# Kernel optimization log

Measured on AMD Instinct MI355X. Metric: run time of the kernel, lower is better.

Reference implementation:

```python
import jax, jax.numpy as jnp
import numpy as np


def _gru_cell(x, h, Wih, Whh):
    # PyTorch GRU (bias=False): gates ordered [r, z, n] along rows of W.
    gi = x @ Wih.T              # [B, 3H]
    gh = h @ Whh.T              # [B, 3H]
    ir, iz, inn = jnp.split(gi, 3, axis=-1)
    hr, hz, hn = jnp.split(gh, 3, axis=-1)
    r = jax.nn.sigmoid(ir + hr)
    z = jax.nn.sigmoid(iz + hz)
    n = jnp.tanh(inn + r * hn)
    return (1.0 - z) * n + z * h


def setup_inputs() -> dict:
    key = jax.random.key(0)
    ks = jax.random.split(key, 16)
    B, T = 256, 1024
    U, Z, Y, H = 16, 16, 16, 128
    W = 0.1  # weight scale for stable recurrence
    inp = {
        "u": jax.random.normal(ks[0], (B, U, T), jnp.float32),
        "y": jax.random.normal(ks[1], (B, Y, T), jnp.float32),
        "h0": jax.random.uniform(ks[2], (2, B, H), jnp.float32),
        "Wih0": W * jax.random.normal(ks[3], (3 * H, U + Z), jnp.float32),
        "Whh0": W * jax.random.normal(ks[4], (3 * H, H), jnp.float32),
        "Wih1": W * jax.random.normal(ks[5], (3 * H, H), jnp.float32),
        "Whh1": W * jax.random.normal(ks[6], (3 * H, H), jnp.float32),
        "dW1": W * jax.random.normal(ks[7], (H, U + H), jnp.float32),
        "db1": jnp.zeros((H,), jnp.float32),
        "dW2": W * jax.random.normal(ks[8], (Z, H), jnp.float32),
        "db2": jnp.zeros((Z,), jnp.float32),
        "mW1": W * jax.random.normal(ks[9], (H, Z + H), jnp.float32),
        "mb1": jnp.zeros((H,), jnp.float32),
        "mW2": W * jax.random.normal(ks[10], (H, H), jnp.float32),
        "mb2": jnp.zeros((H,), jnp.float32),
        "mW3": W * jax.random.normal(ks[11], (Y, H), jnp.float32),
        "mb3": jnp.zeros((Y,), jnp.float32),
    }
    return inp


def reference(u, y, h0, Wih0, Whh0, Wih1, Whh1,
              dW1, db1, dW2, db2, mW1, mb1, mW2, mb2, mW3, mb3):
    B, Z = u.shape[0], dW2.shape[0]
    u_t = jnp.transpose(u, (2, 0, 1))  # [T, B, U]
    y_t = jnp.transpose(y, (2, 0, 1))  # [T, B, Y]

    def step(carry, xs):
        h, x_prev, loss = carry  # h: [2, B, H]
        ut, yt = xs
        inp = jnp.concatenate([ut, x_prev], axis=1)       # [B, U+Z]
        h0n = _gru_cell(inp, h[0], Wih0, Whh0)
        h1n = _gru_cell(h0n, h[1], Wih1, Whh1)
        h_new = jnp.stack([h0n, h1n], axis=0)
        # dynn: two Linears, no activation; input cat(u_t, h[-1])
        d_in = jnp.concatenate([ut, h1n], axis=1)         # [B, U+H]
        x_t = (d_in @ dW1.T + db1) @ dW2.T + db2          # [B, Z]
        # menn: Linear -> ReLU -> Linear -> Linear; input cat(x_t, h[0])
        m_in = jnp.concatenate([x_t, h0n], axis=1)        # [B, Z+H]
        m = jax.nn.relu(m_in @ mW1.T + mb1)
        m = m @ mW2.T + mb2
        y_hat = m @ mW3.T + mb3                           # [B, Y]
        loss = loss + jnp.sum((y_hat - yt) ** 2)
        return (h_new, x_t, loss), None

    x0 = jnp.zeros((B, Z), jnp.float32)  # x_tm1 at t=0 is zeros
    (_, _, loss), _ = jax.lax.scan(step, (h0, x0, jnp.float32(0.0)), (u_t, y_t))
    return loss
```

## Files before the change

kernel.cpp:

```cpp
#include <hip/hip_runtime.h>

typedef __bf16 bf16x8 __attribute__((ext_vector_type(8)));
typedef float f32x4 __attribute__((ext_vector_type(4)));
typedef unsigned int uint32;
typedef unsigned short ushort16_t;

#define T_STEPS 1024
#define CHUNK 32

#define H0_OFF   0
#define H1_OFF   8704
#define M1_OFF   17408
#define XB_OFF   21760
#define ZP_OFF   22528
#define UCH_OFF  22592
#define YCH_OFF  47168
#define WL_OFF   71744
#define LDS_BYTES 146496

#define TG0 0
#define TG1 24
#define TG2 120
#define TG3 216
#define TG4 312
#define TG5 317
#define TG6 357
#define NT_TOT 361
#define SC_DC  369664
#define SC_ME  378880
#define SC_DBC 387072
#define SC_MBE 387136

static __device__ __forceinline__ ushort16_t f2bf(float f) {
    uint32 u = __builtin_bit_cast(uint32, f);
    return (ushort16_t)((u + 0x7FFFu + ((u >> 16) & 1u)) >> 16);
}
static __device__ __forceinline__ float bf2f(ushort16_t h) {
    uint32 u = ((uint32)h) << 16;
    return __builtin_bit_cast(float, u);
}
static __device__ __forceinline__ float sigm(float x) { return 1.f / (1.f + __expf(-x)); }
static __device__ __forceinline__ float tanh_fast(float x) {
    x = fmaxf(fminf(x, 30.f), -30.f);
    float e = __expf(-2.f * x);
    return (1.f - e) / (1.f + e);
}
static __device__ __forceinline__ f32x4 mfma16(bf16x8 a, bf16x8 b, f32x4 c) {
    return __builtin_amdgcn_mfma_f32_16x16x32_bf16(a, b, c, 0, 0, 0);
}
static __device__ __forceinline__ bf16x8 ldsAF(const char* p) {
    return __builtin_bit_cast(bf16x8, *(const uint4*)p);
}

__global__ void prep1(const float* __restrict__ dW1, const float* __restrict__ db1,
                      const float* __restrict__ dW2, const float* __restrict__ db2,
                      const float* __restrict__ mW2, const float* __restrict__ mb2,
                      const float* __restrict__ mW3, const float* __restrict__ mb3,
                      char* __restrict__ ws, float* __restrict__ out) {
    int id = blockIdx.x * 256 + threadIdx.x;
    if (id == 0) *out = 0.f;
    if (id < 2304) {
        int n = id / 144, k = id % 144;
        float s = 0.f;
        for (int h = 0; h < 128; ++h) s += dW2[n * 128 + h] * dW1[h * 144 + k];
        ((float*)(ws + SC_DC))[id] = s;
    } else if (id < 4352) {
        int e = id - 2304, n = e / 128, k = e % 128;
        float s = 0.f;
        for (int h = 0; h < 128; ++h) s += mW3[n * 128 + h] * mW2[h * 128 + k];
        ((float*)(ws + SC_ME))[e] = s;
    } else if (id < 4368) {
        int n = id - 4352;
        float s = db2[n];
        for (int h = 0; h < 128; ++h) s += dW2[n * 128 + h] * db1[h];
        ((float*)(ws + SC_DBC))[n] = s;
    } else if (id < 4384) {
        int n = id - 4368;
        float s = mb3[n];
        for (int h = 0; h < 128; ++h) s += mW3[n * 128 + h] * mb2[h];
        ((float*)(ws + SC_MBE))[n] = s;
    }
}

__global__ void prep2(const float* __restrict__ W0, const float* __restrict__ W1,
                      const float* __restrict__ W2, const float* __restrict__ W3,
                      const float* __restrict__ W5, char* __restrict__ ws) {
    const int tt = blockIdx.x;
    const int lane = threadIdx.x;
    const int cum[8] = {TG0, TG1, TG2, TG3, TG4, TG5, TG6, NT_TOT};
    const int Kreal[7] = {32, 128, 128, 128, 144, 144, 128};
    const int KT[7] = {1, 4, 4, 4, 5, 5, 4};
    const float* Ws[7] = {W0, W1, W2, W3, (const float*)(ws + SC_DC), W5, (const float*)(ws + SC_ME)};
    int g = 0;
    while (tt >= cum[g + 1]) ++g;
    const int tl = tt - cum[g];
    const int kt = tl % KT[g];
    const int n = (tl / KT[g]) * 16 + (lane & 15);
    const float* W = Ws[g];
    ushort16_t* o = (ushort16_t*)ws + tt * 512 + lane * 8;
#pragma unroll
    for (int j = 0; j < 8; ++j) {
        int k = kt * 32 + (lane >> 4) * 8 + j;
        o[j] = (k < Kreal[g]) ? f2bf(W[n * Kreal[g] + k]) : (ushort16_t)0;
    }
}

__global__ __launch_bounds__(512, 2) void rnn_main(
    const float* __restrict__ u, const float* __restrict__ yg, const float* __restrict__ h0g,
    const char* __restrict__ ws, const float* __restrict__ mb1g,
    const float* __restrict__ dbCg, const float* __restrict__ mbEg,
    float* __restrict__ out) {
    __shared__ __align__(16) char smem[LDS_BYTES];
    const int tid = threadIdx.x;
    const int lane = tid & 63;
    const int w = tid >> 6;
    const int lr = lane & 15;
    const int lg = lane >> 4;
    const int r0 = blockIdx.x * 16;
    const uint4* F4 = (const uint4*)ws;
    const f32x4 zero = {0.f, 0.f, 0.f, 0.f};

    for (int i = tid; i < (768 + 64) / 4; i += 512) *(uint32*)(smem + XB_OFF + i * 4) = 0;
    for (int i = tid; i < 1024; i += 512) {
        int lay = i >> 9, rem = i & 511, rr = rem >> 5, k4 = rem & 31;
        float4 v = *(const float4*)(h0g + (lay * 256 + r0 + rr) * 128 + k4 * 4);
        uint2 pk;
        pk.x = (uint32)f2bf(v.x) | ((uint32)f2bf(v.y) << 16);
        pk.y = (uint32)f2bf(v.z) | ((uint32)f2bf(v.w) << 16);
        *(uint2*)(smem + H0_OFF + lay * 8704 + rr * 272 + k4 * 8) = pk;
    }
    for (int i = tid; i < 73 * 64; i += 512) {
        int li = i >> 6, ln2 = i & 63;
        int gt2 = (li < 24) ? li : (li < 29) ? TG4 + (li - 24) : (li < 69) ? TG5 + (li - 29) : TG6 + (li - 69);
        *((uint4*)(smem + WL_OFF) + i) = F4[gt2 * 64 + ln2];
    }
    __syncthreads();

    bf16x8 wW[3][3][4];
    for (int p = 0; p < 6; ++p) {
        for (int i = tid; i < 3072; i += 512)
            *((uint4*)(smem + UCH_OFF) + i) = F4[(TG1 + p * 48) * 64 + i];
        __syncthreads();
#pragma unroll
        for (int mat = 0; mat < 3; ++mat)
#pragma unroll
            for (int gg = 0; gg < 3; ++gg) {
                int rel0 = mat * 96 + gg * 32 + w * 4;
                if (rel0 >= p * 48 && rel0 < p * 48 + 48) {
#pragma unroll
                    for (int kt = 0; kt < 4; ++kt)
                        wW[mat][gg][kt] = ldsAF(smem + UCH_OFF + (rel0 - p * 48 + kt) * 1024 + lane * 16);
                }
            }
        __syncthreads();
    }

    const float mb1_c = mb1g[w * 16 + lr];
    const float dbC_l = dbCg[lr];
    const float mbE_l = mbEg[lr];
    float loss = 0.f;

    const int r = lr;
    for (int t = 0; t <= T_STEPS; ++t) {
        const int cur = t & 1, nxt = cur ^ 1;
        const char* h0c = smem + H0_OFF + cur * 4352;
        char* h0n = smem + H0_OFF + nxt * 4352;
        const char* h1c = smem + H1_OFF + cur * 4352;
        char* h1n = smem + H1_OFF + nxt * 4352;
        const int s = t & (CHUNK - 1);

        if ((t & (CHUNK - 1)) == 0) {
            if (t < T_STEPS) {
                for (int q = 0; q < 16; ++q) {
                    int pair = w * 32 + q * 2 + (lane >> 5);
                    int rr2 = pair >> 4, ch = pair & 15, ss = lane & 31;
                    float v = u[(r0 + rr2) * 16384 + ch * 1024 + t + ss];
                    *(ushort16_t*)(smem + UCH_OFF + ss * 768 + rr2 * 48 + ch * 2) = f2bf(v);
                }
            }
            for (int q = 0; q < 16; ++q) {
                int pair = w * 32 + q * 2 + (lane >> 5);
                int rr2 = pair >> 4, ch = pair & 15, ss = lane & 31;
                int gt = t - 1 + ss;
                if (gt >= 0 && gt < T_STEPS) {
                    float v = yg[(r0 + rr2) * 16384 + ch * 1024 + gt];
                    *(ushort16_t*)(smem + YCH_OFF + ss * 768 + rr2 * 48 + ch * 2) = f2bf(v);
                }
            }
            __syncthreads();
        }

        if (t < T_STEPS) {
            const char* ainp_p = (lg < 2) ? (smem + UCH_OFF + s * 768 + r * 48 + lg * 16)
                                          : (smem + XB_OFF + r * 48 + (lg - 2) * 16);
            bf16x8 a_inp = ldsAF(ainp_p);
            bf16x8 ah[4];
#pragma unroll
            for (int kt = 0; kt < 4; ++kt) ah[kt] = ldsAF(h0c + r * 272 + kt * 64 + lg * 16);
            f32x4 aRi = mfma16(a_inp, ldsAF(smem + WL_OFF + (0 * 8 + w) * 1024 + lane * 16), zero);
            f32x4 aZi = mfma16(a_inp, ldsAF(smem + WL_OFF + (1 * 8 + w) * 1024 + lane * 16), zero);
            f32x4 aNi = mfma16(a_inp, ldsAF(smem + WL_OFF + (2 * 8 + w) * 1024 + lane * 16), zero);
            f32x4 aRh = zero, aZh = zero, aNh = zero;
#pragma unroll
            for (int kt = 0; kt < 4; ++kt) {
                aRh = mfma16(ah[kt], wW[0][0][kt], aRh);
                aZh = mfma16(ah[kt], wW[0][1][kt], aZh);
                aNh = mfma16(ah[kt], wW[0][2][kt], aNh);
            }
            const int c = w * 16 + lr;
#pragma unroll
            for (int i = 0; i < 4; ++i) {
                int row = lg * 4 + i;
                float hold = bf2f(*(const ushort16_t*)(h0c + row * 272 + c * 2));
                float rr = sigm(aRi[i] + aRh[i]);
                float zz = sigm(aZi[i] + aZh[i]);
                float nn = tanh_fast(aNi[i] + rr * aNh[i]);
                *(ushort16_t*)(h0n + row * 272 + c * 2) = f2bf((1.f - zz) * nn + zz * hold);
            }
        }
        if (t > 0) {
            bf16x8 am[5];
            am[0] = ldsAF((lg < 2) ? (smem + XB_OFF + r * 48 + lg * 16) : (h0c + r * 272 + (lg - 2) * 16));
#pragma unroll
            for (int kt = 1; kt < 4; ++kt) am[kt] = ldsAF(h0c + r * 272 + kt * 64 - 32 + lg * 16);
            am[4] = ldsAF((lg < 2) ? (h0c + r * 272 + 224 + lg * 16) : (smem + ZP_OFF + (lg - 2) * 16));
            f32x4 m = zero;
#pragma unroll
            for (int kt = 0; kt < 5; ++kt)
                m = mfma16(am[kt], ldsAF(smem + WL_OFF + (29 + w * 5 + kt) * 1024 + lane * 16), m);
#pragma unroll
            for (int i = 0; i < 4; ++i) {
                int row = lg * 4 + i;
                *(ushort16_t*)(smem + M1_OFF + row * 272 + (w * 16 + lr) * 2) =
                    f2bf(fmaxf(m[i] + mb1_c, 0.f));
            }
        }
        __syncthreads();

        if (t < T_STEPS) {
            bf16x8 ag[4], ahh[4];
#pragma unroll
            for (int kt = 0; kt < 4; ++kt) {
                ag[kt] = ldsAF(h0n + r * 272 + kt * 64 + lg * 16);
                ahh[kt] = ldsAF(h1c + r * 272 + kt * 64 + lg * 16);
            }
            f32x4 bRi = zero, bRh = zero, bZi = zero, bZh = zero, bNi = zero, bNh = zero;
#pragma unroll
            for (int kt = 0; kt < 4; ++kt) {
                bRi = mfma16(ag[kt], wW[1][0][kt], bRi);
                bRh = mfma16(ahh[kt], wW[2][0][kt], bRh);
                bZi = mfma16(ag[kt], wW[1][1][kt], bZi);
                bZh = mfma16(ahh[kt], wW[2][1][kt], bZh);
                bNi = mfma16(ag[kt], wW[1][2][kt], bNi);
                bNh = mfma16(ahh[kt], wW[2][2][kt], bNh);
            }
            const int c = w * 16 + lr;
#pragma unroll
            for (int i = 0; i < 4; ++i) {
                int row = lg * 4 + i;
                float hold = bf2f(*(const ushort16_t*)(h1c + row * 272 + c * 2));
                float rr = sigm(bRi[i] + bRh[i]);
                float zz = sigm(bZi[i] + bZh[i]);
                float nn = tanh_fast(bNi[i] + rr * bNh[i]);
                *(ushort16_t*)(h1n + row * 272 + c * 2) = f2bf((1.f - zz) * nn + zz * hold);
            }
        }
        if (t > 0 && w == 7) {
            bf16x8 am1[4];
#pragma unroll
            for (int kt = 0; kt < 4; ++kt) am1[kt] = ldsAF(smem + M1_OFF + r * 272 + kt * 64 + lg * 16);
            f32x4 acc = zero;
#pragma unroll
            for (int kt = 0; kt < 4; ++kt)
                acc = mfma16(am1[kt], ldsAF(smem + WL_OFF + (69 + kt) * 1024 + lane * 16), acc);
#pragma unroll
            for (int i = 0; i < 4; ++i) {
                int row = lg * 4 + i;
                float yv = bf2f(*(const ushort16_t*)(smem + YCH_OFF + s * 768 + row * 48 + lr * 2));
                float d = acc[i] + mbE_l - yv;
                loss += d * d;
            }
        }
        __syncthreads();

        if (t < T_STEPS && w == 0) {
            bf16x8 ad[5];
            ad[0] = ldsAF((lg < 2) ? (smem + UCH_OFF + s * 768 + r * 48 + lg * 16)
                                   : (h1n + r * 272 + (lg - 2) * 16));
#pragma unroll
            for (int kt = 1; kt < 4; ++kt) ad[kt] = ldsAF(h1n + r * 272 + kt * 64 - 32 + lg * 16);
            ad[4] = ldsAF((lg < 2) ? (h1n + r * 272 + 224 + lg * 16) : (smem + ZP_OFF + (lg - 2) * 16));
            f32x4 acc = zero;
#pragma unroll
            for (int kt = 0; kt < 5; ++kt)
                acc = mfma16(ad[kt], ldsAF(smem + WL_OFF + (24 + kt) * 1024 + lane * 16), acc);
#pragma unroll
            for (int i = 0; i < 4; ++i) {
                int row = lg * 4 + i;
                *(ushort16_t*)(smem + XB_OFF + row * 48 + lr * 2) = f2bf(acc[i] + dbC_l);
            }
        }
        __syncthreads();
    }

    if (w == 7) {
#pragma unroll
        for (int off = 32; off > 0; off >>= 1) loss += __shfl_down(loss, off, 64);
        if (lane == 0) atomicAdd(out, loss);
    }
}

extern "C" void kernel_launch(void* const* d_in, const int* in_sizes, int n_in,
                              void* d_out, int out_size, void* d_ws, size_t ws_size,
                              hipStream_t stream) {
    const float* u    = (const float*)d_in[0];
    const float* y    = (const float*)d_in[1];
    const float* h0   = (const float*)d_in[2];
    const float* Wih0 = (const float*)d_in[3];
    const float* Whh0 = (const float*)d_in[4];
    const float* Wih1 = (const float*)d_in[5];
    const float* Whh1 = (const float*)d_in[6];
    const float* dW1  = (const float*)d_in[7];
    const float* db1  = (const float*)d_in[8];
    const float* dW2  = (const float*)d_in[9];
    const float* db2  = (const float*)d_in[10];
    const float* mW1  = (const float*)d_in[11];
    const float* mb1  = (const float*)d_in[12];
    const float* mW2  = (const float*)d_in[13];
    const float* mb2  = (const float*)d_in[14];
    const float* mW3  = (const float*)d_in[15];
    const float* mb3  = (const float*)d_in[16];
    float* out = (float*)d_out;
    char* ws = (char*)d_ws;

    prep1<<<dim3(18), dim3(256), 0, stream>>>(dW1, db1, dW2, db2, mW2, mb2, mW3, mb3, ws, out);
    prep2<<<dim3(NT_TOT), dim3(64), 0, stream>>>(Wih0, Whh0, Wih1, Whh1, mW1, ws);
    rnn_main<<<dim3(16), dim3(512), 0, stream>>>(u, y, h0, ws, mb1,
                                                 (const float*)(ws + SC_DBC),
                                                 (const float*)(ws + SC_MBE), out);
}
```

Before: 3.327 ms.

## Compute dynn output redundantly per wave via MFMA and lane permute, dropping a barrier

Every wave now recomputes the small dynn projection x_t from the previous h1 with a transposed MFMA and redistributes it through ds_bpermute. This removes the wave-0-only stage and one of the three block barriers per timestep. The menn first layer is moved into the same phase as the layer-0 GRU, and the previous hidden state is kept in fp32 registers instead of being reloaded from LDS. The change also adds faster exp2/rcp sigmoid and tanh, packed bf16 conversion, and split accumulators that shorten MFMA dependency chains. The cost is redundant MFMA work in each wave and an epilogue that handles the final step separately.

```diff
diff --git a/kernel.cpp b/kernel.cpp
--- a/kernel.cpp
+++ b/kernel.cpp
@@ -3,20 +3,17 @@
 typedef __bf16 bf16x8 __attribute__((ext_vector_type(8)));
 typedef float f32x4 __attribute__((ext_vector_type(4)));
 typedef unsigned int uint32;
-typedef unsigned short ushort16_t;
+typedef unsigned short u16;
 
 #define T_STEPS 1024
-#define CHUNK 32
 
 #define H0_OFF   0
 #define H1_OFF   8704
 #define M1_OFF   17408
-#define XB_OFF   21760
-#define ZP_OFF   22528
-#define UCH_OFF  22592
-#define YCH_OFF  47168
-#define WL_OFF   71744
-#define LDS_BYTES 146496
+#define UCH_OFF  21760
+#define YCH_OFF  46336
+#define WL_OFF   70912
+#define LDS_BYTES 145664
 
 #define TG0 0
 #define TG1 24
@@ -31,19 +28,26 @@
 #define SC_DBC 387072
 #define SC_MBE 387136
 
-static __device__ __forceinline__ ushort16_t f2bf(float f) {
+static __device__ __forceinline__ u16 f2bf(float f) {
     uint32 u = __builtin_bit_cast(uint32, f);
-    return (ushort16_t)((u + 0x7FFFu + ((u >> 16) & 1u)) >> 16);
-}
-static __device__ __forceinline__ float bf2f(ushort16_t h) {
+    return (u16)((u + 0x7FFFu + ((u >> 16) & 1u)) >> 16);
+}
+static __device__ __forceinline__ float bf2f(u16 h) {
     uint32 u = ((uint32)h) << 16;
     return __builtin_bit_cast(float, u);
 }
-static __device__ __forceinline__ float sigm(float x) { return 1.f / (1.f + __expf(-x)); }
+static __device__ __forceinline__ uint32 cvtpk(float a, float b) {
+    uint32 r;
+    asm("v_cvt_pk_bf16_f32 %0, %1, %2" : "=v"(r) : "v"(a), "v"(b));
+    return r;
+}
+static __device__ __forceinline__ float sigm(float x) {
+    return __builtin_amdgcn_rcpf(1.f + __builtin_amdgcn_exp2f(x * -1.4426950408889634f));
+}
 static __device__ __forceinline__ float tanh_fast(float x) {
-    x = fmaxf(fminf(x, 30.f), -30.f);
-    float e = __expf(-2.f * x);
-    return (1.f - e) / (1.f + e);
+    float xm = fmaxf(x, -30.f);
+    float e = __builtin_amdgcn_exp2f(xm * -2.8853900817779268f);
+    return fmaf(2.f, __builtin_amdgcn_rcpf(e + 1.f), -1.f);
 }
 static __device__ __forceinline__ f32x4 mfma16(bf16x8 a, bf16x8 b, f32x4 c) {
     return __builtin_amdgcn_mfma_f32_16x16x32_bf16(a, b, c, 0, 0, 0);
@@ -97,11 +101,11 @@
     const int kt = tl % KT[g];
     const int n = (tl / KT[g]) * 16 + (lane & 15);
     const float* W = Ws[g];
-    ushort16_t* o = (ushort16_t*)ws + tt * 512 + lane * 8;
+    u16* o = (u16*)ws + tt * 512 + lane * 8;
 #pragma unroll
     for (int j = 0; j < 8; ++j) {
         int k = kt * 32 + (lane >> 4) * 8 + j;
-        o[j] = (k < Kreal[g]) ? f2bf(W[n * Kreal[g] + k]) : (ushort16_t)0;
+        o[j] = (k < Kreal[g]) ? f2bf(W[n * Kreal[g] + k]) : (u16)0;
     }
 }
 
@@ -119,8 +123,8 @@
     const int r0 = blockIdx.x * 16;
     const uint4* F4 = (const uint4*)ws;
     const f32x4 zero = {0.f, 0.f, 0.f, 0.f};
-
-    for (int i = tid; i < (768 + 64) / 4; i += 512) *(uint32*)(smem + XB_OFF + i * 4) = 0;
+    const bf16x8 z8 = __builtin_bit_cast(bf16x8, (uint4){0u, 0u, 0u, 0u});
+
     for (int i = tid; i < 1024; i += 512) {
         int lay = i >> 9, rem = i & 511, rr = rem >> 5, k4 = rem & 31;
         float4 v = *(const float4*)(h0g + (lay * 256 + r0 + rr) * 128 + k4 * 4);
@@ -156,27 +160,56 @@
     }
 
     const float mb1_c = mb1g[w * 16 + lr];
-    const float dbC_l = dbCg[lr];
     const float mbE_l = mbEg[lr];
+    float dbc4[4];
+#pragma unroll
+    for (int i = 0; i < 4; ++i) dbc4[i] = dbCg[lg * 4 + i];
+    float hp0[4], hp1[4];
+#pragma unroll
+    for (int i = 0; i < 4; ++i) {
+        hp0[i] = h0g[(r0 + lg * 4 + i) * 128 + w * 16 + lr];
+        hp1[i] = h0g[(256 + r0 + lg * 4 + i) * 128 + w * 16 + lr];
+    }
     float loss = 0.f;
-
-    const int r = lr;
-    for (int t = 0; t <= T_STEPS; ++t) {
-        const int cur = t & 1, nxt = cur ^ 1;
-        const char* h0c = smem + H0_OFF + cur * 4352;
-        char* h0n = smem + H0_OFF + nxt * 4352;
-        const char* h1c = smem + H1_OFF + cur * 4352;
-        char* h1n = smem + H1_OFF + nxt * 4352;
-        const int s = t & (CHUNK - 1);
-
-        if ((t & (CHUNK - 1)) == 0) {
-            if (t < T_STEPS) {
-                for (int q = 0; q < 16; ++q) {
-                    int pair = w * 32 + q * 2 + (lane >> 5);
-                    int rr2 = pair >> 4, ch = pair & 15, ss = lane & 31;
-                    float v = u[(r0 + rr2) * 16384 + ch * 1024 + t + ss];
-                    *(ushort16_t*)(smem + UCH_OFF + ss * 768 + rr2 * 48 + ch * 2) = f2bf(v);
-                }
+    const int c2 = (w * 16 + lr) * 2;
+    const int bp0 = (lr + (lg & 1) * 32) * 4;
+
+    for (int t = 0; t < T_STEPS; ++t) {
+        const char* h0c = smem + H0_OFF + (t & 1) * 4352;
+        char* h0n = smem + H0_OFF + ((t & 1) ^ 1) * 4352;
+        const char* h1c = smem + H1_OFF + (t & 1) * 4352;
+        char* h1n = smem + H1_OFF + ((t & 1) ^ 1) * 4352;
+        const int s = t & 31, sp = (t - 1) & 31;
+
+        const char* h1r = h1c + lr * 272;
+        bf16x8 ad0 = ldsAF((lg < 2) ? (smem + UCH_OFF + sp * 768 + lr * 48 + lg * 16)
+                                    : (h1r + (lg - 2) * 16));
+        bf16x8 ad1 = ldsAF(h1r + 32 + lg * 16);
+        bf16x8 ad2 = ldsAF(h1r + 96 + lg * 16);
+        bf16x8 ad3 = ldsAF(h1r + 160 + lg * 16);
+        bf16x8 ad4t = ldsAF(h1r + 224 + (lg & 1) * 16);
+        bf16x8 ad4 = (lg < 2) ? ad4t : z8;
+        f32x4 xa = mfma16(ldsAF(smem + WL_OFF + 24 * 1024 + lane * 16), ad0, zero);
+        xa = mfma16(ldsAF(smem + WL_OFF + 25 * 1024 + lane * 16), ad1, xa);
+        xa = mfma16(ldsAF(smem + WL_OFF + 26 * 1024 + lane * 16), ad2, xa);
+        f32x4 xb = mfma16(ldsAF(smem + WL_OFF + 27 * 1024 + lane * 16), ad3, zero);
+        xb = mfma16(ldsAF(smem + WL_OFF + 28 * 1024 + lane * 16), ad4, xb);
+        uint32 pk0 = cvtpk(xa[0] + xb[0] + dbc4[0], xa[1] + xb[1] + dbc4[1]);
+        uint32 pk1 = cvtpk(xa[2] + xb[2] + dbc4[2], xa[3] + xb[3] + dbc4[3]);
+        if (t == 0) { pk0 = 0u; pk1 = 0u; }
+        uint32 d0 = (uint32)__builtin_amdgcn_ds_bpermute(bp0, (int)pk0);
+        uint32 d1 = (uint32)__builtin_amdgcn_ds_bpermute(bp0, (int)pk1);
+        uint32 d2 = (uint32)__builtin_amdgcn_ds_bpermute(bp0 + 64, (int)pk0);
+        uint32 d3 = (uint32)__builtin_amdgcn_ds_bpermute(bp0 + 64, (int)pk1);
+        bf16x8 xfrag = __builtin_bit_cast(bf16x8, (uint4){d0, d1, d2, d3});
+
+        if ((t & 31) == 0) {
+            __syncthreads();
+            for (int q = 0; q < 16; ++q) {
+                int pair = w * 32 + q * 2 + (lane >> 5);
+                int rr2 = pair >> 4, ch = pair & 15, ss = lane & 31;
+                float v = u[(r0 + rr2) * 16384 + ch * 1024 + t + ss];
+                *(u16*)(smem + UCH_OFF + ss * 768 + rr2 * 48 + ch * 2) = f2bf(v);
             }
             for (int q = 0; q < 16; ++q) {
                 int pair = w * 32 + q * 2 + (lane >> 5);
@@ -184,123 +217,186 @@
                 int gt = t - 1 + ss;
                 if (gt >= 0 && gt < T_STEPS) {
                     float v = yg[(r0 + rr2) * 16384 + ch * 1024 + gt];
-                    *(ushort16_t*)(smem + YCH_OFF + ss * 768 + rr2 * 48 + ch * 2) = f2bf(v);
+                    *(u16*)(smem + YCH_OFF + ss * 768 + rr2 * 48 + ch * 2) = f2bf(v);
                 }
             }
             __syncthreads();
         }
 
-        if (t < T_STEPS) {
-            const char* ainp_p = (lg < 2) ? (smem + UCH_OFF + s * 768 + r * 48 + lg * 16)
-                                          : (smem + XB_OFF + r * 48 + (lg - 2) * 16);
-            bf16x8 a_inp = ldsAF(ainp_p);
-            bf16x8 ah[4];
-#pragma unroll
-            for (int kt = 0; kt < 4; ++kt) ah[kt] = ldsAF(h0c + r * 272 + kt * 64 + lg * 16);
-            f32x4 aRi = mfma16(a_inp, ldsAF(smem + WL_OFF + (0 * 8 + w) * 1024 + lane * 16), zero);
-            f32x4 aZi = mfma16(a_inp, ldsAF(smem + WL_OFF + (1 * 8 + w) * 1024 + lane * 16), zero);
-            f32x4 aNi = mfma16(a_inp, ldsAF(smem + WL_OFF + (2 * 8 + w) * 1024 + lane * 16), zero);
-            f32x4 aRh = zero, aZh = zero, aNh = zero;
-#pragma unroll
-            for (int kt = 0; kt < 4; ++kt) {
-                aRh = mfma16(ah[kt], wW[0][0][kt], aRh);
-                aZh = mfma16(ah[kt], wW[0][1][kt], aZh);
-                aNh = mfma16(ah[kt], wW[0][2][kt], aNh);
+        bf16x8 ufrag = ldsAF(smem + UCH_OFF + s * 768 + lr * 48 + (lg & 1) * 16);
+        bf16x8 a_inp = (lg < 2) ? ufrag : xfrag;
+        const char* h0r = h0c + lr * 272;
+        bf16x8 ah0 = ldsAF(h0r + lg * 16);
+        bf16x8 ah1 = ldsAF(h0r + 64 + lg * 16);
+        bf16x8 ah2 = ldsAF(h0r + 128 + lg * 16);
+        bf16x8 ah3 = ldsAF(h0r + 192 + lg * 16);
+        bf16x8 b0r = ldsAF(smem + WL_OFF + (0 * 8 + w) * 1024 + lane * 16);
+        bf16x8 b0z = ldsAF(smem + WL_OFF + (1 * 8 + w) * 1024 + lane * 16);
+        bf16x8 b0n = ldsAF(smem + WL_OFF + (2 * 8 + w) * 1024 + lane * 16);
+        f32x4 rA = mfma16(ah0, wW[0][0][0], zero);
+        rA = mfma16(ah1, wW[0][0][1], rA);
+        rA = mfma16(a_inp, b0r, rA);
+        f32x4 rB = mfma16(ah2, wW[0][0][2], zero);
+        rB = mfma16(ah3, wW[0][0][3], rB);
+        f32x4 zA = mfma16(ah0, wW[0][1][0], zero);
+        zA = mfma16(ah1, wW[0][1][1], zA);
+        zA = mfma16(a_inp, b0z, zA);
+        f32x4 zB = mfma16(ah2, wW[0][1][2], zero);
+        zB = mfma16(ah3, wW[0][1][3], zB);
+        f32x4 nI = mfma16(a_inp, b0n, zero);
+        f32x4 nA = mfma16(ah0, wW[0][2][0], zero);
+        nA = mfma16(ah1, wW[0][2][1], nA);
+        f32x4 nB = mfma16(ah2, wW[0][2][2], zero);
+        nB = mfma16(ah3, wW[0][2][3], nB);
+        bf16x8 t0 = ldsAF(h0r + (lg & 1) * 16);
+        bf16x8 am0 = (lg < 2) ? xfrag : t0;
+        bf16x8 am1 = ldsAF(h0r + 32 + lg * 16);
+        bf16x8 am2 = ldsAF(h0r + 96 + lg * 16);
+        bf16x8 am3 = ldsAF(h0r + 160 + lg * 16);
+        bf16x8 am4t = ldsAF(h0r + 224 + (lg & 1) * 16);
+        bf16x8 am4 = (lg < 2) ? am4t : z8;
+        f32x4 mA = mfma16(am1, ldsAF(smem + WL_OFF + (29 + w * 5 + 1) * 1024 + lane * 16), zero);
+        mA = mfma16(am2, ldsAF(smem + WL_OFF + (29 + w * 5 + 2) * 1024 + lane * 16), mA);
+        mA = mfma16(am0, ldsAF(smem + WL_OFF + (29 + w * 5 + 0) * 1024 + lane * 16), mA);
+        f32x4 mB = mfma16(am3, ldsAF(smem + WL_OFF + (29 + w * 5 + 3) * 1024 + lane * 16), zero);
+        mB = mfma16(am4, ldsAF(smem + WL_OFF + (29 + w * 5 + 4) * 1024 + lane * 16), mB);
+#pragma unroll
+        for (int i = 0; i < 4; ++i) {
+            float rr = sigm(rA[i] + rB[i]);
+            float zz = sigm(zA[i] + zB[i]);
+            float nn = tanh_fast(fmaf(rr, nA[i] + nB[i], nI[i]));
+            float hnew = fmaf(zz, hp0[i] - nn, nn);
+            hp0[i] = hnew;
+            *(u16*)(h0n + (lg * 4 + i) * 272 + c2) = (u16)cvtpk(hnew, hnew);
+            float mv = fmaxf(mA[i] + mB[i] + mb1_c, 0.f);
+            *(u16*)(smem + M1_OFF + (lg * 4 + i) * 272 + c2) = (u16)cvtpk(mv, mv);
+        }
+        __syncthreads();
+
+        const char* h0nr = h0n + lr * 272;
+        bf16x8 ag0 = ldsAF(h0nr + lg * 16);
+        bf16x8 ag1 = ldsAF(h0nr + 64 + lg * 16);
+        bf16x8 ag2 = ldsAF(h0nr + 128 + lg * 16);
+        bf16x8 ag3 = ldsAF(h0nr + 192 + lg * 16);
+        bf16x8 av0 = ldsAF(h1r + lg * 16);
+        bf16x8 av1 = ldsAF(h1r + 64 + lg * 16);
+        bf16x8 av2 = ldsAF(h1r + 128 + lg * 16);
+        bf16x8 av3 = ldsAF(h1r + 192 + lg * 16);
+        f32x4 RA = mfma16(ag0, wW[1][0][0], zero);
+        RA = mfma16(ag1, wW[1][0][1], RA);
+        RA = mfma16(ag2, wW[1][0][2], RA);
+        RA = mfma16(ag3, wW[1][0][3], RA);
+        f32x4 RB = mfma16(av0, wW[2][0][0], zero);
+        RB = mfma16(av1, wW[2][0][1], RB);
+        RB = mfma16(av2, wW[2][0][2], RB);
+        RB = mfma16(av3, wW[2][0][3], RB);
+        f32x4 ZA = mfma16(ag0, wW[1][1][0], zero);
+        ZA = mfma16(ag1, wW[1][1][1], ZA);
+        ZA = mfma16(ag2, wW[1][1][2], ZA);
+        ZA = mfma16(ag3, wW[1][1][3], ZA);
+        f32x4 ZB = mfma16(av0, wW[2][1][0], zero);
+        ZB = mfma16(av1, wW[2][1][1], ZB);
+        ZB = mfma16(av2, wW[2][1][2], ZB);
+        ZB = mfma16(av3, wW[2][1][3], ZB);
+        f32x4 NI = mfma16(ag0, wW[1][2][0], zero);
+        NI = mfma16(ag1, wW[1][2][1], NI);
+        NI = mfma16(ag2, wW[1][2][2], NI);
+        NI = mfma16(ag3, wW[1][2][3], NI);
+        f32x4 NH = mfma16(av0, wW[2][2][0], zero);
+        NH = mfma16(av1, wW[2][2][1], NH);
+        NH = mfma16(av2, wW[2][2][2], NH);
+        NH = mfma16(av3, wW[2][2][3], NH);
+#pragma unroll
+        for (int i = 0; i < 4; ++i) {
+            float rr = sigm(RA[i] + RB[i]);
+            float zz = sigm(ZA[i] + ZB[i]);
+            float nn = tanh_fast(fmaf(rr, NH[i], NI[i]));
+            float hnew = fmaf(zz, hp1[i] - nn, nn);
+            hp1[i] = hnew;
+            *(u16*)(h1n + (lg * 4 + i) * 272 + c2) = (u16)cvtpk(hnew, hnew);
+        }
+        if (w == 7) {
+            const char* m1r = smem + M1_OFF + lr * 272;
+            bf16x8 q0 = ldsAF(m1r + lg * 16);
+            bf16x8 q1 = ldsAF(m1r + 64 + lg * 16);
+            bf16x8 q2 = ldsAF(m1r + 128 + lg * 16);
+            bf16x8 q3 = ldsAF(m1r + 192 + lg * 16);
+            f32x4 lA = mfma16(q0, ldsAF(smem + WL_OFF + 69 * 1024 + lane * 16), zero);
+            lA = mfma16(q1, ldsAF(smem + WL_OFF + 70 * 1024 + lane * 16), lA);
+            f32x4 lB = mfma16(q2, ldsAF(smem + WL_OFF + 71 * 1024 + lane * 16), zero);
+            lB = mfma16(q3, ldsAF(smem + WL_OFF + 72 * 1024 + lane * 16), lB);
+            const float gd = (t > 0) ? 1.f : 0.f;
+#pragma unroll
+            for (int i = 0; i < 4; ++i) {
+                float yh = lA[i] + lB[i] + mbE_l;
+                float yv = bf2f(*(const u16*)(smem + YCH_OFF + s * 768 + (lg * 4 + i) * 48 + lr * 2));
+                float d = yh - yv;
+                loss = fmaf(gd * d, d, loss);
             }
-            const int c = w * 16 + lr;
+        }
+        __syncthreads();
+    }
+
+    {
+        const char* h0c = smem + H0_OFF;
+        const char* h1c = smem + H1_OFF;
+        const char* h1r = h1c + lr * 272;
+        const char* h0r = h0c + lr * 272;
+        bf16x8 ad0 = ldsAF((lg < 2) ? (smem + UCH_OFF + 31 * 768 + lr * 48 + lg * 16)
+                                    : (h1r + (lg - 2) * 16));
+        bf16x8 ad1 = ldsAF(h1r + 32 + lg * 16);
+        bf16x8 ad2 = ldsAF(h1r + 96 + lg * 16);
+        bf16x8 ad3 = ldsAF(h1r + 160 + lg * 16);
+        bf16x8 ad4t = ldsAF(h1r + 224 + (lg & 1) * 16);
+        bf16x8 ad4 = (lg < 2) ? ad4t : z8;
+        f32x4 xa = mfma16(ldsAF(smem + WL_OFF + 24 * 1024 + lane * 16), ad0, zero);
+        xa = mfma16(ldsAF(smem + WL_OFF + 25 * 1024 + lane * 16), ad1, xa);
+        xa = mfma16(ldsAF(smem + WL_OFF + 26 * 1024 + lane * 16), ad2, xa);
+        f32x4 xb = mfma16(ldsAF(smem + WL_OFF + 27 * 1024 + lane * 16), ad3, zero);
+        xb = mfma16(ldsAF(smem + WL_OFF + 28 * 1024 + lane * 16), ad4, xb);
+        uint32 pk0 = cvtpk(xa[0] + xb[0] + dbc4[0], xa[1] + xb[1] + dbc4[1]);
+        uint32 pk1 = cvtpk(xa[2] + xb[2] + dbc4[2], xa[3] + xb[3] + dbc4[3]);
+        uint32 d0 = (uint32)__builtin_amdgcn_ds_bpermute(bp0, (int)pk0);
+        uint32 d1 = (uint32)__builtin_amdgcn_ds_bpermute(bp0, (int)pk1);
+        uint32 d2 = (uint32)__builtin_amdgcn_ds_bpermute(bp0 + 64, (int)pk0);
+        uint32 d3 = (uint32)__builtin_amdgcn_ds_bpermute(bp0 + 64, (int)pk1);
+        bf16x8 xfrag = __builtin_bit_cast(bf16x8, (uint4){d0, d1, d2, d3});
+        bf16x8 t0 = ldsAF(h0r + (lg & 1) * 16);
+        bf16x8 am0 = (lg < 2) ? xfrag : t0;
+        bf16x8 am1 = ldsAF(h0r + 32 + lg * 16);
+        bf16x8 am2 = ldsAF(h0r + 96 + lg * 16);
+        bf16x8 am3 = ldsAF(h0r + 160 + lg * 16);
+        bf16x8 am4t = ldsAF(h0r + 224 + (lg & 1) * 16);
+        bf16x8 am4 = (lg < 2) ? am4t : z8;
+        f32x4 mA = mfma16(am0, ldsAF(smem + WL_OFF + (29 + w * 5 + 0) * 1024 + lane * 16), zero);
+        mA = mfma16(am1, ldsAF(smem + WL_OFF + (29 + w * 5 + 1) * 1024 + lane * 16), mA);
+        mA = mfma16(am2, ldsAF(smem + WL_OFF + (29 + w * 5 + 2) * 1024 + lane * 16), mA);
+        f32x4 mB = mfma16(am3, ldsAF(smem + WL_OFF + (29 + w * 5 + 3) * 1024 + lane * 16), zero);
+        mB = mfma16(am4, ldsAF(smem + WL_OFF + (29 + w * 5 + 4) * 1024 + lane * 16), mB);
+#pragma unroll
+        for (int i = 0; i < 4; ++i) {
+            float mv = fmaxf(mA[i] + mB[i] + mb1_c, 0.f);
+            *(u16*)(smem + M1_OFF + (lg * 4 + i) * 272 + c2) = (u16)cvtpk(mv, mv);
+        }
+        __syncthreads();
+        if (w == 7) {
+            const char* m1r = smem + M1_OFF + lr * 272;
+            bf16x8 q0 = ldsAF(m1r + lg * 16);
+            bf16x8 q1 = ldsAF(m1r + 64 + lg * 16);
+            bf16x8 q2 = ldsAF(m1r + 128 + lg * 16);
+            bf16x8 q3 = ldsAF(m1r + 192 + lg * 16);
+            f32x4 lA = mfma16(q0, ldsAF(smem + WL_OFF + 69 * 1024 + lane * 16), zero);
+            lA = mfma16(q1, ldsAF(smem + WL_OFF + 70 * 1024 + lane * 16), lA);
+            f32x4 lB = mfma16(q2, ldsAF(smem + WL_OFF + 71 * 1024 + lane * 16), zero);
+            lB = mfma16(q3, ldsAF(smem + WL_OFF + 72 * 1024 + lane * 16), lB);
 #pragma unroll
             for (int i = 0; i < 4; ++i) {
-                int row = lg * 4 + i;
-                float hold = bf2f(*(const ushort16_t*)(h0c + row * 272 + c * 2));
-                float rr = sigm(aRi[i] + aRh[i]);
-                float zz = sigm(aZi[i] + aZh[i]);
-                float nn = tanh_fast(aNi[i] + rr * aNh[i]);
-                *(ushort16_t*)(h0n + row * 272 + c * 2) = f2bf((1.f - zz) * nn + zz * hold);
+                float yh = lA[i] + lB[i] + mbE_l;
+                float yv = yg[(r0 + lg * 4 + i) * 16384 + lr * 1024 + 1023];
+                float d = yh - yv;
+                loss = fmaf(d, d, loss);
             }
         }
-        if (t > 0) {
-            bf16x8 am[5];
-            am[0] = ldsAF((lg < 2) ? (smem + XB_OFF + r * 48 + lg * 16) : (h0c + r * 272 + (lg - 2) * 16));
-#pragma unroll
-            for (int kt = 1; kt < 4; ++kt) am[kt] = ldsAF(h0c + r * 272 + kt * 64 - 32 + lg * 16);
-            am[4] = ldsAF((lg < 2) ? (h0c + r * 272 + 224 + lg * 16) : (smem + ZP_OFF + (lg - 2) * 16));
-            f32x4 m = zero;
-#pragma unroll
-            for (int kt = 0; kt < 5; ++kt)
-                m = mfma16(am[kt], ldsAF(smem + WL_OFF + (29 + w * 5 + kt) * 1024 + lane * 16), m);
-#pragma unroll
-            for (int i = 0; i < 4; ++i) {
-                int row = lg * 4 + i;
-                *(ushort16_t*)(smem + M1_OFF + row * 272 + (w * 16 + lr) * 2) =
-                    f2bf(fmaxf(m[i] + mb1_c, 0.f));
-            }
-        }
-        __syncthreads();
-
-        if (t < T_STEPS) {
-            bf16x8 ag[4], ahh[4];
-#pragma unroll
-            for (int kt = 0; kt < 4; ++kt) {
-                ag[kt] = ldsAF(h0n + r * 272 + kt * 64 + lg * 16);
-                ahh[kt] = ldsAF(h1c + r * 272 + kt * 64 + lg * 16);
-            }
-            f32x4 bRi = zero, bRh = zero, bZi = zero, bZh = zero, bNi = zero, bNh = zero;
-#pragma unroll
-            for (int kt = 0; kt < 4; ++kt) {
-                bRi = mfma16(ag[kt], wW[1][0][kt], bRi);
-                bRh = mfma16(ahh[kt], wW[2][0][kt], bRh);
-                bZi = mfma16(ag[kt], wW[1][1][kt], bZi);
-                bZh = mfma16(ahh[kt], wW[2][1][kt], bZh);
-                bNi = mfma16(ag[kt], wW[1][2][kt], bNi);
-                bNh = mfma16(ahh[kt], wW[2][2][kt], bNh);
-            }
-            const int c = w * 16 + lr;
-#pragma unroll
-            for (int i = 0; i < 4; ++i) {
-                int row = lg * 4 + i;
-                float hold = bf2f(*(const ushort16_t*)(h1c + row * 272 + c * 2));
-                float rr = sigm(bRi[i] + bRh[i]);
-                float zz = sigm(bZi[i] + bZh[i]);
-                float nn = tanh_fast(bNi[i] + rr * bNh[i]);
-                *(ushort16_t*)(h1n + row * 272 + c * 2) = f2bf((1.f - zz) * nn + zz * hold);
-            }
-        }
-        if (t > 0 && w == 7) {
-            bf16x8 am1[4];
-#pragma unroll
-            for (int kt = 0; kt < 4; ++kt) am1[kt] = ldsAF(smem + M1_OFF + r * 272 + kt * 64 + lg * 16);
-            f32x4 acc = zero;
-#pragma unroll
-            for (int kt = 0; kt < 4; ++kt)
-                acc = mfma16(am1[kt], ldsAF(smem + WL_OFF + (69 + kt) * 1024 + lane * 16), acc);
-#pragma unroll
-            for (int i = 0; i < 4; ++i) {
-                int row = lg * 4 + i;
-                float yv = bf2f(*(const ushort16_t*)(smem + YCH_OFF + s * 768 + row * 48 + lr * 2));
-                float d = acc[i] + mbE_l - yv;
-                loss += d * d;
-            }
-        }
-        __syncthreads();
-
-        if (t < T_STEPS && w == 0) {
-            bf16x8 ad[5];
-            ad[0] = ldsAF((lg < 2) ? (smem + UCH_OFF + s * 768 + r * 48 + lg * 16)
-                                   : (h1n + r * 272 + (lg - 2) * 16));
-#pragma unroll
-            for (int kt = 1; kt < 4; ++kt) ad[kt] = ldsAF(h1n + r * 272 + kt * 64 - 32 + lg * 16);
-            ad[4] = ldsAF((lg < 2) ? (h1n + r * 272 + 224 + lg * 16) : (smem + ZP_OFF + (lg - 2) * 16));
-            f32x4 acc = zero;
-#pragma unroll
-            for (int kt = 0; kt < 5; ++kt)
-                acc = mfma16(ad[kt], ldsAF(smem + WL_OFF + (24 + kt) * 1024 + lane * 16), acc);
-#pragma unroll
-            for (int i = 0; i < 4; ++i) {
-                int row = lg * 4 + i;
-                *(ushort16_t*)(smem + XB_OFF + row * 48 + lr * 2) = f2bf(acc[i] + dbC_l);
-            }
-        }
-        __syncthreads();
     }
 
     if (w == 7) {
```

New measurement: 2.778 ms. 1.2x faster.
